# Optimization experiments

Measured on AMD Instinct MI355X. Metric: run time of the kernel, lower is better.

The kernel has to match this reference:

```python
import jax, jax.numpy as jnp
import numpy as np

SH_DEGREE = 4
SH_DIM = (SH_DEGREE + 1) ** 2  # 25
SCALE_MIN, SCALE_MAX = 0.01, 100.0
SCALE_PCT = 0.1
SRF, GPP = 1, 1


def sh_basis(d):
    # Real spherical harmonics up to l=4 for unit directions d (..., 3) -> (..., 25)
    x, y, z = d[..., 0], d[..., 1], d[..., 2]
    x2, y2, z2 = x * x, y * y, z * z
    return jnp.stack([
        jnp.full_like(x, 0.2820947918),
        0.4886025119 * y, 0.4886025119 * z, 0.4886025119 * x,
        1.0925484306 * x * y, 1.0925484306 * y * z, 0.3153915653 * (3.0 * z2 - 1.0),
        1.0925484306 * x * z, 0.5462742153 * (x2 - y2),
        0.5900435899 * y * (3.0 * x2 - y2), 2.8906114426 * x * y * z,
        0.4570457995 * y * (5.0 * z2 - 1.0), 0.3731763326 * z * (5.0 * z2 - 3.0),
        0.4570457995 * x * (5.0 * z2 - 1.0), 1.4453057213 * z * (x2 - y2),
        0.5900435899 * x * (x2 - 3.0 * y2),
        2.5033429418 * x * y * (x2 - y2), 1.7701307698 * y * z * (3.0 * x2 - y2),
        0.9461746958 * x * y * (7.0 * z2 - 1.0), 0.6690465436 * y * z * (7.0 * z2 - 3.0),
        0.1057855469 * (35.0 * z2 * z2 - 30.0 * z2 + 3.0),
        0.6690465436 * x * z * (7.0 * z2 - 3.0),
        0.4730873479 * (x2 - y2) * (7.0 * z2 - 1.0),
        1.7701307698 * x * z * (x2 - 3.0 * y2),
        0.6258357354 * (x2 * x2 - 6.0 * x2 * y2 + y2 * y2),
    ], -1)


# Fixed sample directions + inverse basis matrices for per-band SH rotation (Wigner-D via sampling)
_rng = np.random.default_rng(0)
_SAMPLES, _YS_INV = {}, {}
for _l in range(1, SH_DEGREE + 1):
    _v = _rng.normal(size=(2 * _l + 1, 3))
    _v /= np.linalg.norm(_v, axis=-1, keepdims=True)
    _SAMPLES[_l] = _v.astype(np.float32)
    _B = np.asarray(sh_basis(jnp.asarray(_SAMPLES[_l])))[:, _l * _l:(_l + 1) ** 2]  # (n, n) rows=samples
    _YS_INV[_l] = np.linalg.inv(_B.T).astype(np.float32)  # inverse of columns-are-samples matrix


def quat_to_rotmat(q):
    # wxyz convention
    w, x, y, z = q[..., 0], q[..., 1], q[..., 2], q[..., 3]
    r0 = jnp.stack([1 - 2 * (y * y + z * z), 2 * (x * y - w * z), 2 * (x * z + w * y)], -1)
    r1 = jnp.stack([2 * (x * y + w * z), 1 - 2 * (x * x + z * z), 2 * (y * z - w * x)], -1)
    r2 = jnp.stack([2 * (x * z - w * y), 2 * (y * z + w * x), 1 - 2 * (x * x + y * y)], -1)
    return jnp.stack([r0, r1, r2], -2)


def rotate_sh(sh, R_c2w):
    # sh: (B,V,R,srf,gpp,3,25); R_c2w: (B,V,3,3). Block-diagonal per-band rotation.
    outs = [sh[..., :1]]  # l=0 invariant
    for l in range(1, SH_DEGREE + 1):
        lo, hi = l * l, (l + 1) ** 2
        S = jnp.asarray(_SAMPLES[l])  # (n,3)
        drot = jnp.einsum('bvji,nj->bvni', R_c2w, S)  # R^T d_n
        Yrot = jnp.swapaxes(sh_basis(drot)[..., lo:hi], -1, -2)  # (B,V,n,n) columns=samples
        D = jnp.swapaxes(Yrot @ jnp.asarray(_YS_INV[l]), -1, -2)  # coefficient rotation
        outs.append(jnp.einsum('bvmn,bvrsgxn->bvrsgxm', D, sh[..., lo:hi]))
    return jnp.concatenate(outs, -1)


def setup_inputs() -> dict:
    key = jax.random.key(0)
    ks = jax.random.split(key, 8)
    B, V, H, W = 2, 4, 256, 256
    R = H * W
    C = 3 + 4 + 3 * SH_DIM  # 82
    pre_gaussians = jax.random.normal(ks[0], (B, V, R, SRF, C), jnp.float32)
    pixel_centers = jax.random.uniform(ks[1], (B, V, R, SRF, 2), jnp.float32)
    q = jax.random.normal(ks[2], (B, V, 4), jnp.float32)
    q = q / jnp.linalg.norm(q, axis=-1, keepdims=True)
    Rm = quat_to_rotmat(q)
    t = 0.5 * jax.random.normal(ks[3], (B, V, 3), jnp.float32)
    E = jnp.zeros((B, V, 4, 4), jnp.float32)
    E = E.at[..., :3, :3].set(Rm).at[..., :3, 3].set(t).at[..., 3, 3].set(1.0)
    f = 1.0 + 0.2 * jax.random.uniform(ks[4], (B, V, 2), jnp.float32)
    c = 0.5 + 0.02 * jax.random.normal(ks[5], (B, V, 2), jnp.float32)
    K = jnp.zeros((B, V, 3, 3), jnp.float32)
    K = K.at[..., 0, 0].set(f[..., 0]).at[..., 1, 1].set(f[..., 1])
    K = K.at[..., 0, 2].set(c[..., 0]).at[..., 1, 2].set(c[..., 1]).at[..., 2, 2].set(1.0)
    opacities = jax.random.uniform(ks[6], (B, V, R), jnp.float32)
    depths = 0.5 + 9.5 * jax.random.uniform(ks[7], (B, V, R), jnp.float32)
    return {"pre_gaussians": pre_gaussians, "pixel_centers": pixel_centers,
            "extrinsics": E, "intrinsics": K, "opacities": opacities,
            "depths": depths, "img_h": H, "img_w": W}


def reference(pre_gaussians, pixel_centers, extrinsics, intrinsics, opacities, depths, img_h, img_w):
    H, W = img_h, img_w
    B, V, R = pre_gaussians.shape[:3]
    C = pre_gaussians.shape[-1]
    pg = jnp.broadcast_to(pre_gaussians[..., None, :], (B, V, R, SRF, GPP, C))
    pc = jnp.broadcast_to(pixel_centers[..., None, :], (B, V, R, SRF, GPP, 2))
    op = jnp.broadcast_to(opacities[..., None, None], (B, V, R, SRF, GPP))
    dep = jnp.broadcast_to(depths[..., None, None], (B, V, R, SRF, GPP))
    scales_raw, quats, sh = pg[..., :3], pg[..., 3:7], pg[..., 7:]
    scales = (SCALE_MIN + (SCALE_MAX - SCALE_MIN) * jax.nn.sigmoid(scales_raw)) * dep[..., None]
    pixel_size = jnp.array([1.0 / W, 1.0 / H], jnp.float32)
    K2inv = jnp.linalg.inv(intrinsics[..., :2, :2])
    scale_adj = SCALE_PCT * jnp.einsum('bvij,j->bv', K2inv, pixel_size)
    scales = scales * scale_adj[:, :, None, None, None, None]
    quats = quats / jnp.linalg.norm(quats, axis=-1, keepdims=True)
    R_w2c = extrinsics[..., :3, :3]
    R_c2w = jnp.swapaxes(R_w2c, -1, -2)
    Rq = quat_to_rotmat(quats)
    cov = jnp.einsum('...ik,...k,...jk->...ij', Rq, scales * scales, Rq)  # Rq S S^T Rq^T
    cov = jnp.einsum('bvai,bvrsgij,bvcj->bvrsgac', R_c2w, cov, R_c2w)
    Kinv = jnp.linalg.inv(intrinsics)
    xy1 = jnp.concatenate([pc, jnp.ones_like(pc[..., :1])], -1)
    dir_cam = jnp.einsum('bvij,bvrsgj->bvrsgi', Kinv, xy1)
    dir_cam = dir_cam / jnp.linalg.norm(dir_cam, axis=-1, keepdims=True)
    ray_d = jnp.einsum('bvij,bvrsgj->bvrsgi', R_c2w, dir_cam)
    t = extrinsics[..., :3, 3]
    cam_o = -jnp.einsum('bvij,bvj->bvi', R_c2w, t)  # camera center in world
    ray_o = jnp.broadcast_to(cam_o[:, :, None, None, None, :], ray_d.shape)
    means = ray_o + ray_d * dep[..., None]
    sh = sh.reshape(B, V, R, SRF, GPP, 3, SH_DIM)
    sh = rotate_sh(sh, R_c2w)
    return (means, scales, cov, quats, op, sh)
```

## Files before the change

kernel.cpp:

```cpp
#include <hip/hip_runtime.h>

#define VSZ  192
#define TILE 64
#define NTHR 256
#define IN_F  (TILE * 82)
#define SEC_M  0
#define SEC_S  192
#define SEC_C  384
#define SEC_Q  960
#define SEC_O  1216
#define SEC_SH 1280
#define OUT_F  6080

__device__ __forceinline__ void sh_basis25(float x, float y, float z, float* Y) {
    float x2 = x * x, y2 = y * y, z2 = z * z;
    Y[0]  = 0.2820947918f;
    Y[1]  = 0.4886025119f * y;
    Y[2]  = 0.4886025119f * z;
    Y[3]  = 0.4886025119f * x;
    Y[4]  = 1.0925484306f * x * y;
    Y[5]  = 1.0925484306f * y * z;
    Y[6]  = 0.3153915653f * (3.0f * z2 - 1.0f);
    Y[7]  = 1.0925484306f * x * z;
    Y[8]  = 0.5462742153f * (x2 - y2);
    Y[9]  = 0.5900435899f * y * (3.0f * x2 - y2);
    Y[10] = 2.8906114426f * x * y * z;
    Y[11] = 0.4570457995f * y * (5.0f * z2 - 1.0f);
    Y[12] = 0.3731763326f * z * (5.0f * z2 - 3.0f);
    Y[13] = 0.4570457995f * x * (5.0f * z2 - 1.0f);
    Y[14] = 1.4453057213f * z * (x2 - y2);
    Y[15] = 0.5900435899f * x * (x2 - 3.0f * y2);
    Y[16] = 2.5033429418f * x * y * (x2 - y2);
    Y[17] = 1.7701307698f * y * z * (3.0f * x2 - y2);
    Y[18] = 0.9461746958f * x * y * (7.0f * z2 - 1.0f);
    Y[19] = 0.6690465436f * y * z * (7.0f * z2 - 3.0f);
    Y[20] = 0.1057855469f * (35.0f * z2 * z2 - 30.0f * z2 + 3.0f);
    Y[21] = 0.6690465436f * x * z * (7.0f * z2 - 3.0f);
    Y[22] = 0.4730873479f * (x2 - y2) * (7.0f * z2 - 1.0f);
    Y[23] = 1.7701307698f * x * z * (x2 - 3.0f * y2);
    Y[24] = 0.6258357354f * (x2 * x2 - 6.0f * x2 * y2 + y2 * y2);
}

__global__ __launch_bounds__(64) void setup_kernel(
        const float* __restrict__ ext,
        const float* __restrict__ intr,
        const int* __restrict__ ph,
        const int* __restrict__ pw,
        float* __restrict__ vdg) {
    __shared__ float Bs[24][9];
    __shared__ float Yrs[24][9];
    __shared__ float normInv[24];

    int bv = blockIdx.x;
    int tid = threadIdx.x;
    const float* E = ext + bv * 16;
    const float* K = intr + bv * 9;
    float* o = vdg + bv * VSZ;

    const float z0 = 0.5f, r0 = 0.8660254037844386f;
    const float TWO_PI = 6.283185307179586f;

    if (tid < 24) {
        int l, base;
        if      (tid < 3)  { l = 1; base = 0;  }
        else if (tid < 8)  { l = 2; base = 3;  }
        else if (tid < 15) { l = 3; base = 8;  }
        else               { l = 4; base = 15; }
        int n  = 2 * l + 1;
        int si = tid - base;
        int lo = l * l;
        float phs = 0.4f + TWO_PI * (float)si / (float)n;
        float sx = r0 * cosf(phs), sy = r0 * sinf(phs), sz = z0;
        float Y[25];
        sh_basis25(sx, sy, sz, Y);
        for (int k = 0; k < n; k++) Bs[tid][k] = Y[lo + k];
        float dx = E[0] * sx + E[1] * sy + E[2]  * sz;
        float dy = E[4] * sx + E[5] * sy + E[6]  * sz;
        float dz = E[8] * sx + E[9] * sy + E[10] * sz;
        sh_basis25(dx, dy, dz, Y);
        for (int k = 0; k < n; k++) Yrs[tid][k] = Y[lo + k];
    }
    __syncthreads();

    if (tid < 24) {
        int l, base;
        if      (tid < 3)  { l = 1; base = 0;  }
        else if (tid < 8)  { l = 2; base = 3;  }
        else if (tid < 15) { l = 3; base = 8;  }
        else               { l = 4; base = 15; }
        int n = 2 * l + 1;
        int m = tid - base;
        float acc = 0.f;
        for (int s = 0; s < n; s++) { float v = Bs[base + s][m]; acc += v * v; }
        normInv[tid] = 1.0f / acc;
    }
    __syncthreads();

    const int dofs[5] = {0, 22, 31, 56, 105};
    for (int e = tid; e < 164; e += 64) {
        int l, ebase, sbase;
        if      (e < 9)  { l = 1; ebase = 0;  sbase = 0;  }
        else if (e < 34) { l = 2; ebase = 9;  sbase = 3;  }
        else if (e < 83) { l = 3; ebase = 34; sbase = 8;  }
        else             { l = 4; ebase = 83; sbase = 15; }
        int n = 2 * l + 1;
        int el = e - ebase;
        int m = el / n, k = el % n;
        float acc = 0.f;
        for (int s = 0; s < n; s++) acc += Yrs[sbase + s][k] * Bs[sbase + s][m];
        o[dofs[l] + m * n + k] = acc * normInv[sbase + m];
    }

    if (tid == 0) {
        float Rw2c[3][3], Rc2w[3][3], t[3];
        for (int i = 0; i < 3; i++) {
            for (int j = 0; j < 3; j++) Rw2c[i][j] = E[i * 4 + j];
            t[i] = E[i * 4 + 3];
        }
        for (int i = 0; i < 3; i++)
            for (int j = 0; j < 3; j++) Rc2w[i][j] = Rw2c[j][i];
        for (int i = 0; i < 3; i++)
            for (int j = 0; j < 3; j++) o[i * 3 + j] = Rc2w[i][j];
        for (int i = 0; i < 3; i++) {
            float s = 0.f;
            for (int j = 0; j < 3; j++) s += Rc2w[i][j] * t[j];
            o[9 + i] = -s;
        }
        float a = K[0], b = K[1], c = K[2], d = K[3], e = K[4], f = K[5],
              g = K[6], h = K[7], ii = K[8];
        float det = a * (e * ii - f * h) - b * (d * ii - f * g) + c * (d * h - e * g);
        float id = 1.0f / det;
        o[12 + 0] = (e * ii - f * h) * id; o[12 + 1] = (c * h - b * ii) * id; o[12 + 2] = (b * f - c * e) * id;
        o[12 + 3] = (f * g - d * ii) * id; o[12 + 4] = (a * ii - c * g) * id; o[12 + 5] = (c * d - a * f) * id;
        o[12 + 6] = (d * h - e * g) * id; o[12 + 7] = (b * g - a * h) * id; o[12 + 8] = (a * e - b * d) * id;
        float det2 = a * e - b * d;
        float i00 = e / det2, i01 = -b / det2, i10 = -d / det2, i11 = a / det2;
        float ps0 = 1.0f / (float)(*pw), ps1 = 1.0f / (float)(*ph);
        o[21] = 0.1f * ((i00 + i10) * ps0 + (i01 + i11) * ps1);
    }
}

template <int NB>
__device__ __forceinline__ void apply_D(const float* __restrict__ D,
                                        const float* __restrict__ si,
                                        float* __restrict__ so) {
#pragma unroll
    for (int m = 0; m < NB; m++) {
        float acc = 0.f;
#pragma unroll
        for (int k = 0; k < NB; k++) acc += D[m * NB + k] * si[k];
        so[m] = acc;
    }
}

__global__ __launch_bounds__(NTHR, 6) void adapter_kernel(
    const float* __restrict__ pg, const float* __restrict__ pc,
    const float* __restrict__ ops, const float* __restrict__ deps,
    const float* __restrict__ vdg, float* __restrict__ out,
    int R, long long N)
{
    __shared__ __align__(16) float tile[OUT_F];
    __shared__ float vd[VSZ];

    int bv = blockIdx.y;
    long long tilebase = (long long)bv * R + (long long)blockIdx.x * TILE;
    int cnt = R - blockIdx.x * TILE;
    if (cnt > TILE) cnt = TILE;
    bool full = (cnt == TILE);

    for (int i = threadIdx.x; i < 186; i += NTHR) vd[i] = vdg[bv * VSZ + i];

    const float* src = pg + tilebase * 82;
    if (full) {
        const float4* s4 = (const float4*)src;
        float4* t4 = (float4*)tile;
        for (int e = threadIdx.x; e < IN_F / 4; e += NTHR) t4[e] = s4[e];
    } else {
        for (int ff = threadIdx.x; ff < cnt * 82; ff += NTHR) tile[ff] = src[ff];
    }
    __syncthreads();

    int rec = threadIdx.x & 63;
    int sub = threadIdx.x >> 6;
    bool active = rec < cnt;
    long long g = tilebase + rec;
    const float* row = tile + rec * 82;

    float gin[7];
    float depth = 0.f, opac = 0.f, px = 0.f, py = 0.f;
    float si[25];

    if (sub == 0) {
        if (active) {
#pragma unroll
            for (int i = 0; i < 7; i++) gin[i] = row[i];
            depth = deps[g];
            opac  = ops[g];
            float2 pxy = ((const float2*)pc)[g];
            px = pxy.x; py = pxy.y;
        }
    } else {
        if (active) {
            int cb = 7 + 25 * (sub - 1);
#pragma unroll
            for (int m = 0; m < 25; m++) si[m] = row[cb + m];
        }
    }
    __syncthreads();

    if (sub == 0) {
        if (active) {
            float sadj = vd[21];
            float sc[3];
#pragma unroll
            for (int i = 0; i < 3; i++) {
                float sg = 1.0f / (1.0f + expf(-gin[i]));
                sc[i] = (0.01f + 99.99f * sg) * depth * sadj;
            }
            float qw = gin[3], qx = gin[4], qy = gin[5], qz = gin[6];
            float qn = rsqrtf(qw * qw + qx * qx + qy * qy + qz * qz);
            qw *= qn; qx *= qn; qy *= qn; qz *= qn;
            float Rq[3][3];
            Rq[0][0] = 1.f - 2.f * (qy * qy + qz * qz);
            Rq[0][1] = 2.f * (qx * qy - qw * qz);
            Rq[0][2] = 2.f * (qx * qz + qw * qy);
            Rq[1][0] = 2.f * (qx * qy + qw * qz);
            Rq[1][1] = 1.f - 2.f * (qx * qx + qz * qz);
            Rq[1][2] = 2.f * (qy * qz - qw * qx);
            Rq[2][0] = 2.f * (qx * qz - qw * qy);
            Rq[2][1] = 2.f * (qy * qz + qw * qx);
            Rq[2][2] = 1.f - 2.f * (qx * qx + qy * qy);

            float Rc[3][3];
#pragma unroll
            for (int i = 0; i < 3; i++)
#pragma unroll
                for (int j = 0; j < 3; j++) Rc[i][j] = vd[i * 3 + j];

            float A[3][3];
#pragma unroll
            for (int i = 0; i < 3; i++)
#pragma unroll
                for (int k = 0; k < 3; k++)
                    A[i][k] = Rc[i][0] * Rq[0][k] + Rc[i][1] * Rq[1][k] + Rc[i][2] * Rq[2][k];
            float s2[3] = {sc[0] * sc[0], sc[1] * sc[1], sc[2] * sc[2]};

            float dx = vd[12] * px + vd[13] * py + vd[14];
            float dy = vd[15] * px + vd[16] * py + vd[17];
            float dz = vd[18] * px + vd[19] * py + vd[20];
            float dn = rsqrtf(dx * dx + dy * dy + dz * dz);
            dx *= dn; dy *= dn; dz *= dn;
            float rdx = Rc[0][0] * dx + Rc[0][1] * dy + Rc[0][2] * dz;
            float rdy = Rc[1][0] * dx + Rc[1][1] * dy + Rc[1][2] * dz;
            float rdz = Rc[2][0] * dx + Rc[2][1] * dy + Rc[2][2] * dz;

            tile[SEC_M + 3 * rec + 0] = vd[9]  + rdx * depth;
            tile[SEC_M + 3 * rec + 1] = vd[10] + rdy * depth;
            tile[SEC_M + 3 * rec + 2] = vd[11] + rdz * depth;
            tile[SEC_S + 3 * rec + 0] = sc[0];
            tile[SEC_S + 3 * rec + 1] = sc[1];
            tile[SEC_S + 3 * rec + 2] = sc[2];
#pragma unroll
            for (int i = 0; i < 3; i++)
#pragma unroll
                for (int j = 0; j < 3; j++)
                    tile[SEC_C + 9 * rec + i * 3 + j] =
                        A[i][0] * s2[0] * A[j][0] + A[i][1] * s2[1] * A[j][1] + A[i][2] * s2[2] * A[j][2];
            ((float4*)(tile + SEC_Q))[rec] = make_float4(qw, qx, qy, qz);
            tile[SEC_O + rec] = opac;
        }
    } else {
        if (active) {
            float so[25];
            so[0] = si[0];
            apply_D<3>(vd + 22,  si + 1,  so + 1);
            apply_D<5>(vd + 31,  si + 4,  so + 4);
            apply_D<7>(vd + 56,  si + 9,  so + 9);
            apply_D<9>(vd + 105, si + 16, so + 16);
            float* dstsh = tile + SEC_SH + 75 * rec + 25 * (sub - 1);
#pragma unroll
            for (int m = 0; m < 25; m++) dstsh[m] = so[m];
        }
    }
    __syncthreads();

    if (full) {
        const float4* t4 = (const float4*)tile;
        float4* dm  = (float4*)(out +           3 * tilebase);
        float4* ds  = (float4*)(out +  3 * N +  3 * tilebase);
        float4* dc  = (float4*)(out +  6 * N +  9 * tilebase);
        float4* dq  = (float4*)(out + 15 * N +  4 * tilebase);
        float4* dop = (float4*)(out + 19 * N +      tilebase);
        float4* dsh = (float4*)(out + 20 * N + 75 * tilebase);
        int tid = threadIdx.x;
        if (tid < 48)  dm[tid]  = t4[SEC_M / 4 + tid];
        if (tid < 48)  ds[tid]  = t4[SEC_S / 4 + tid];
        for (int e = tid; e < 144; e += NTHR) dc[e] = t4[SEC_C / 4 + e];
        if (tid < 64)  dq[tid]  = t4[SEC_Q / 4 + tid];
        if (tid < 16)  dop[tid] = t4[SEC_O / 4 + tid];
        for (int e = tid; e < 1200; e += NTHR) dsh[e] = t4[SEC_SH / 4 + e];
    } else {
        int tid = threadIdx.x;
        float* dm  = out +           3 * tilebase;
        float* ds  = out +  3 * N +  3 * tilebase;
        float* dc  = out +  6 * N +  9 * tilebase;
        float* dq  = out + 15 * N +  4 * tilebase;
        float* dop = out + 19 * N +      tilebase;
        float* dsh = out + 20 * N + 75 * tilebase;
        for (int e = tid; e < cnt * 3;  e += NTHR) dm[e]  = tile[SEC_M + e];
        for (int e = tid; e < cnt * 3;  e += NTHR) ds[e]  = tile[SEC_S + e];
        for (int e = tid; e < cnt * 9;  e += NTHR) dc[e]  = tile[SEC_C + e];
        for (int e = tid; e < cnt * 4;  e += NTHR) dq[e]  = tile[SEC_Q + e];
        for (int e = tid; e < cnt;      e += NTHR) dop[e] = tile[SEC_O + e];
        for (int e = tid; e < cnt * 75; e += NTHR) dsh[e] = tile[SEC_SH + e];
    }
}

extern "C" void kernel_launch(void* const* d_in, const int* in_sizes, int n_in,
                              void* d_out, int out_size, void* d_ws, size_t ws_size,
                              hipStream_t stream) {
    const float* pg   = (const float*)d_in[0];
    const float* pc   = (const float*)d_in[1];
    const float* ext  = (const float*)d_in[2];
    const float* intr = (const float*)d_in[3];
    const float* ops  = (const float*)d_in[4];
    const float* dep  = (const float*)d_in[5];
    const int*   ph   = (const int*)d_in[6];
    const int*   pw   = (const int*)d_in[7];

    int BV = in_sizes[2] / 16;
    long long N = (long long)in_sizes[4];
    int R = (int)(N / BV);

    float* vd = (float*)d_ws;
    setup_kernel<<<BV, 64, 0, stream>>>(ext, intr, ph, pw, vd);

    dim3 grid((R + TILE - 1) / TILE, BV);
    adapter_kernel<<<grid, NTHR, 0, stream>>>(pg, pc, ops, dep, vd, (float*)d_out, R, N);
}
```

Baseline: 93.84 us.

## Make blocks persistent over four tiles with async global-to-LDS prefetch

Each block now processes four consecutive tiles. The next tile's input is fetched straight into LDS with global_load_lds while the current tile is computed and written out, and the input and output staging buffers are separated so the prefetch cannot clobber results. The intent is to hide global load latency and cut block launch count. In exchange the grid is four times smaller, which lowers parallelism, and LDS per block grows, which may reduce occupancy.

```diff
diff --git a/kernel.cpp b/kernel.cpp
--- a/kernel.cpp
+++ b/kernel.cpp
@@ -1,8 +1,10 @@
 #include <hip/hip_runtime.h>
+#include <stdint.h>
 
 #define VSZ  192
 #define TILE 64
 #define NTHR 256
+#define NT   4
 #define IN_F  (TILE * 82)
 #define SEC_M  0
 #define SEC_S  192
@@ -11,6 +13,12 @@
 #define SEC_O  1216
 #define SEC_SH 1280
 #define OUT_F  6080
+
+typedef const __attribute__((address_space(1))) uint32_t* gas_ptr;
+typedef __attribute__((address_space(3))) uint32_t* las_ptr;
+__device__ __forceinline__ void g2lds16(const float4* g, float4* l) {
+    __builtin_amdgcn_global_load_lds((gas_ptr)(const void*)g, (las_ptr)(void*)l, 16, 0, 0);
+}
 
 __device__ __forceinline__ void sh_basis25(float x, float y, float z, float* Y) {
     float x2 = x * x, y2 = y * y, z2 = z * z;
@@ -153,166 +161,198 @@
     }
 }
 
-__global__ __launch_bounds__(NTHR, 6) void adapter_kernel(
+__global__ __launch_bounds__(NTHR) void adapter_kernel(
     const float* __restrict__ pg, const float* __restrict__ pc,
     const float* __restrict__ ops, const float* __restrict__ deps,
     const float* __restrict__ vdg, float* __restrict__ out,
-    int R, long long N)
+    int R, long long N, int tilesPerView)
 {
-    __shared__ __align__(16) float tile[OUT_F];
+    __shared__ __align__(16) float inb[IN_F];
+    __shared__ __align__(16) float ob[OUT_F];
     __shared__ float vd[VSZ];
 
     int bv = blockIdx.y;
-    long long tilebase = (long long)bv * R + (long long)blockIdx.x * TILE;
-    int cnt = R - blockIdx.x * TILE;
-    if (cnt > TILE) cnt = TILE;
-    bool full = (cnt == TILE);
+    int t0 = blockIdx.x * NT;
+    if (t0 >= tilesPerView) return;
 
     for (int i = threadIdx.x; i < 186; i += NTHR) vd[i] = vdg[bv * VSZ + i];
 
-    const float* src = pg + tilebase * 82;
-    if (full) {
-        const float4* s4 = (const float4*)src;
-        float4* t4 = (float4*)tile;
-        for (int e = threadIdx.x; e < IN_F / 4; e += NTHR) t4[e] = s4[e];
-    } else {
-        for (int ff = threadIdx.x; ff < cnt * 82; ff += NTHR) tile[ff] = src[ff];
-    }
-    __syncthreads();
-
-    int rec = threadIdx.x & 63;
-    int sub = threadIdx.x >> 6;
-    bool active = rec < cnt;
-    long long g = tilebase + rec;
-    const float* row = tile + rec * 82;
-
-    float gin[7];
-    float depth = 0.f, opac = 0.f, px = 0.f, py = 0.f;
-    float si[25];
-
-    if (sub == 0) {
-        if (active) {
-#pragma unroll
-            for (int i = 0; i < 7; i++) gin[i] = row[i];
-            depth = deps[g];
-            opac  = ops[g];
-            float2 pxy = ((const float2*)pc)[g];
-            px = pxy.x; py = pxy.y;
-        }
-    } else {
-        if (active) {
-            int cb = 7 + 25 * (sub - 1);
-#pragma unroll
-            for (int m = 0; m < 25; m++) si[m] = row[cb + m];
-        }
-    }
-    __syncthreads();
-
-    if (sub == 0) {
-        if (active) {
-            float sadj = vd[21];
-            float sc[3];
-#pragma unroll
-            for (int i = 0; i < 3; i++) {
-                float sg = 1.0f / (1.0f + expf(-gin[i]));
-                sc[i] = (0.01f + 99.99f * sg) * depth * sadj;
-            }
-            float qw = gin[3], qx = gin[4], qy = gin[5], qz = gin[6];
-            float qn = rsqrtf(qw * qw + qx * qx + qy * qy + qz * qz);
-            qw *= qn; qx *= qn; qy *= qn; qz *= qn;
-            float Rq[3][3];
-            Rq[0][0] = 1.f - 2.f * (qy * qy + qz * qz);
-            Rq[0][1] = 2.f * (qx * qy - qw * qz);
-            Rq[0][2] = 2.f * (qx * qz + qw * qy);
-            Rq[1][0] = 2.f * (qx * qy + qw * qz);
-            Rq[1][1] = 1.f - 2.f * (qx * qx + qz * qz);
-            Rq[1][2] = 2.f * (qy * qz - qw * qx);
-            Rq[2][0] = 2.f * (qx * qz - qw * qy);
-            Rq[2][1] = 2.f * (qy * qz + qw * qx);
-            Rq[2][2] = 1.f - 2.f * (qx * qx + qy * qy);
-
-            float Rc[3][3];
-#pragma unroll
-            for (int i = 0; i < 3; i++)
-#pragma unroll
-                for (int j = 0; j < 3; j++) Rc[i][j] = vd[i * 3 + j];
-
-            float A[3][3];
-#pragma unroll
-            for (int i = 0; i < 3; i++)
-#pragma unroll
-                for (int k = 0; k < 3; k++)
-                    A[i][k] = Rc[i][0] * Rq[0][k] + Rc[i][1] * Rq[1][k] + Rc[i][2] * Rq[2][k];
-            float s2[3] = {sc[0] * sc[0], sc[1] * sc[1], sc[2] * sc[2]};
-
-            float dx = vd[12] * px + vd[13] * py + vd[14];
-            float dy = vd[15] * px + vd[16] * py + vd[17];
-            float dz = vd[18] * px + vd[19] * py + vd[20];
-            float dn = rsqrtf(dx * dx + dy * dy + dz * dz);
-            dx *= dn; dy *= dn; dz *= dn;
-            float rdx = Rc[0][0] * dx + Rc[0][1] * dy + Rc[0][2] * dz;
-            float rdy = Rc[1][0] * dx + Rc[1][1] * dy + Rc[1][2] * dz;
-            float rdz = Rc[2][0] * dx + Rc[2][1] * dy + Rc[2][2] * dz;
-
-            tile[SEC_M + 3 * rec + 0] = vd[9]  + rdx * depth;
-            tile[SEC_M + 3 * rec + 1] = vd[10] + rdy * depth;
-            tile[SEC_M + 3 * rec + 2] = vd[11] + rdz * depth;
-            tile[SEC_S + 3 * rec + 0] = sc[0];
-            tile[SEC_S + 3 * rec + 1] = sc[1];
-            tile[SEC_S + 3 * rec + 2] = sc[2];
-#pragma unroll
-            for (int i = 0; i < 3; i++)
-#pragma unroll
-                for (int j = 0; j < 3; j++)
-                    tile[SEC_C + 9 * rec + i * 3 + j] =
-                        A[i][0] * s2[0] * A[j][0] + A[i][1] * s2[1] * A[j][1] + A[i][2] * s2[2] * A[j][2];
-            ((float4*)(tile + SEC_Q))[rec] = make_float4(qw, qx, qy, qz);
-            tile[SEC_O + rec] = opac;
-        }
-    } else {
-        if (active) {
-            float so[25];
-            so[0] = si[0];
-            apply_D<3>(vd + 22,  si + 1,  so + 1);
-            apply_D<5>(vd + 31,  si + 4,  so + 4);
-            apply_D<7>(vd + 56,  si + 9,  so + 9);
-            apply_D<9>(vd + 105, si + 16, so + 16);
-            float* dstsh = tile + SEC_SH + 75 * rec + 25 * (sub - 1);
-#pragma unroll
-            for (int m = 0; m < 25; m++) dstsh[m] = so[m];
-        }
-    }
-    __syncthreads();
-
-    if (full) {
-        const float4* t4 = (const float4*)tile;
-        float4* dm  = (float4*)(out +           3 * tilebase);
-        float4* ds  = (float4*)(out +  3 * N +  3 * tilebase);
-        float4* dc  = (float4*)(out +  6 * N +  9 * tilebase);
-        float4* dq  = (float4*)(out + 15 * N +  4 * tilebase);
-        float4* dop = (float4*)(out + 19 * N +      tilebase);
-        float4* dsh = (float4*)(out + 20 * N + 75 * tilebase);
-        int tid = threadIdx.x;
-        if (tid < 48)  dm[tid]  = t4[SEC_M / 4 + tid];
-        if (tid < 48)  ds[tid]  = t4[SEC_S / 4 + tid];
-        for (int e = tid; e < 144; e += NTHR) dc[e] = t4[SEC_C / 4 + e];
-        if (tid < 64)  dq[tid]  = t4[SEC_Q / 4 + tid];
-        if (tid < 16)  dop[tid] = t4[SEC_O / 4 + tid];
-        for (int e = tid; e < 1200; e += NTHR) dsh[e] = t4[SEC_SH / 4 + e];
-    } else {
-        int tid = threadIdx.x;
-        float* dm  = out +           3 * tilebase;
-        float* ds  = out +  3 * N +  3 * tilebase;
-        float* dc  = out +  6 * N +  9 * tilebase;
-        float* dq  = out + 15 * N +  4 * tilebase;
-        float* dop = out + 19 * N +      tilebase;
-        float* dsh = out + 20 * N + 75 * tilebase;
-        for (int e = tid; e < cnt * 3;  e += NTHR) dm[e]  = tile[SEC_M + e];
-        for (int e = tid; e < cnt * 3;  e += NTHR) ds[e]  = tile[SEC_S + e];
-        for (int e = tid; e < cnt * 9;  e += NTHR) dc[e]  = tile[SEC_C + e];
-        for (int e = tid; e < cnt * 4;  e += NTHR) dq[e]  = tile[SEC_Q + e];
-        for (int e = tid; e < cnt;      e += NTHR) dop[e] = tile[SEC_O + e];
-        for (int e = tid; e < cnt * 75; e += NTHR) dsh[e] = tile[SEC_SH + e];
+    {
+        long long tb = (long long)bv * R + (long long)t0 * TILE;
+        int c = R - t0 * TILE; if (c > TILE) c = TILE;
+        const float* src = pg + tb * 82;
+        if (c == TILE) {
+            const float4* s4 = (const float4*)src;
+            float4* i4 = (float4*)inb;
+            int tid = threadIdx.x;
+#pragma unroll
+            for (int k = 0; k < 5; k++) { int e = k * NTHR + tid; g2lds16(s4 + e, i4 + e); }
+            if (tid < IN_F / 4 - 5 * NTHR) { int e = 5 * NTHR + tid; g2lds16(s4 + e, i4 + e); }
+        } else {
+            for (int ff = threadIdx.x; ff < c * 82; ff += NTHR) inb[ff] = src[ff];
+        }
+    }
+
+    for (int it = 0; it < NT; it++) {
+        int t = t0 + it;
+        if (t >= tilesPerView) break;
+        long long tilebase = (long long)bv * R + (long long)t * TILE;
+        int cnt = R - t * TILE; if (cnt > TILE) cnt = TILE;
+        bool full = (cnt == TILE);
+
+        asm volatile("s_waitcnt vmcnt(0)" ::: "memory");
+        __syncthreads();
+
+        int rec = threadIdx.x & 63;
+        int sub = threadIdx.x >> 6;
+        bool active = rec < cnt;
+        long long g = tilebase + rec;
+        const float* row = inb + rec * 82;
+
+        float gin[7];
+        float depth = 0.f, opac = 0.f, px = 0.f, py = 0.f;
+        float si[25];
+
+        if (sub == 0) {
+            if (active) {
+#pragma unroll
+                for (int i = 0; i < 7; i++) gin[i] = row[i];
+                depth = deps[g];
+                opac  = ops[g];
+                float2 pxy = ((const float2*)pc)[g];
+                px = pxy.x; py = pxy.y;
+            }
+        } else {
+            if (active) {
+                int cb = 7 + 25 * (sub - 1);
+#pragma unroll
+                for (int m = 0; m < 25; m++) si[m] = row[cb + m];
+            }
+        }
+        __syncthreads();
+
+        if (it + 1 < NT && t + 1 < tilesPerView) {
+            long long tb = (long long)bv * R + (long long)(t + 1) * TILE;
+            int c = R - (t + 1) * TILE; if (c > TILE) c = TILE;
+            const float* src = pg + tb * 82;
+            if (c == TILE) {
+                const float4* s4 = (const float4*)src;
+                float4* i4 = (float4*)inb;
+                int tid = threadIdx.x;
+#pragma unroll
+                for (int k = 0; k < 5; k++) { int e = k * NTHR + tid; g2lds16(s4 + e, i4 + e); }
+                if (tid < IN_F / 4 - 5 * NTHR) { int e = 5 * NTHR + tid; g2lds16(s4 + e, i4 + e); }
+            } else {
+                for (int ff = threadIdx.x; ff < c * 82; ff += NTHR) inb[ff] = src[ff];
+            }
+        }
+
+        if (sub == 0) {
+            if (active) {
+                float sadj = vd[21];
+                float sc[3];
+#pragma unroll
+                for (int i = 0; i < 3; i++) {
+                    float sg = 1.0f / (1.0f + expf(-gin[i]));
+                    sc[i] = (0.01f + 99.99f * sg) * depth * sadj;
+                }
+                float qw = gin[3], qx = gin[4], qy = gin[5], qz = gin[6];
+                float qn = rsqrtf(qw * qw + qx * qx + qy * qy + qz * qz);
+                qw *= qn; qx *= qn; qy *= qn; qz *= qn;
+                float Rq[3][3];
+                Rq[0][0] = 1.f - 2.f * (qy * qy + qz * qz);
+                Rq[0][1] = 2.f * (qx * qy - qw * qz);
+                Rq[0][2] = 2.f * (qx * qz + qw * qy);
+                Rq[1][0] = 2.f * (qx * qy + qw * qz);
+                Rq[1][1] = 1.f - 2.f * (qx * qx + qz * qz);
+                Rq[1][2] = 2.f * (qy * qz - qw * qx);
+                Rq[2][0] = 2.f * (qx * qz - qw * qy);
+                Rq[2][1] = 2.f * (qy * qz + qw * qx);
+                Rq[2][2] = 1.f - 2.f * (qx * qx + qy * qy);
+
+                float Rc[3][3];
+#pragma unroll
+                for (int i = 0; i < 3; i++)
+#pragma unroll
+                    for (int j = 0; j < 3; j++) Rc[i][j] = vd[i * 3 + j];
+
+                float A[3][3];
+#pragma unroll
+                for (int i = 0; i < 3; i++)
+#pragma unroll
+                    for (int k = 0; k < 3; k++)
+                        A[i][k] = Rc[i][0] * Rq[0][k] + Rc[i][1] * Rq[1][k] + Rc[i][2] * Rq[2][k];
+                float s2[3] = {sc[0] * sc[0], sc[1] * sc[1], sc[2] * sc[2]};
+
+                float dx = vd[12] * px + vd[13] * py + vd[14];
+                float dy = vd[15] * px + vd[16] * py + vd[17];
+                float dz = vd[18] * px + vd[19] * py + vd[20];
+                float dn = rsqrtf(dx * dx + dy * dy + dz * dz);
+                dx *= dn; dy *= dn; dz *= dn;
+                float rdx = Rc[0][0] * dx + Rc[0][1] * dy + Rc[0][2] * dz;
+                float rdy = Rc[1][0] * dx + Rc[1][1] * dy + Rc[1][2] * dz;
+                float rdz = Rc[2][0] * dx + Rc[2][1] * dy + Rc[2][2] * dz;
+
+                ob[SEC_M + 3 * rec + 0] = vd[9]  + rdx * depth;
+                ob[SEC_M + 3 * rec + 1] = vd[10] + rdy * depth;
+                ob[SEC_M + 3 * rec + 2] = vd[11] + rdz * depth;
+                ob[SEC_S + 3 * rec + 0] = sc[0];
+                ob[SEC_S + 3 * rec + 1] = sc[1];
+                ob[SEC_S + 3 * rec + 2] = sc[2];
+#pragma unroll
+                for (int i = 0; i < 3; i++)
+#pragma unroll
+                    for (int j = 0; j < 3; j++)
+                        ob[SEC_C + 9 * rec + i * 3 + j] =
+                            A[i][0] * s2[0] * A[j][0] + A[i][1] * s2[1] * A[j][1] + A[i][2] * s2[2] * A[j][2];
+                ((float4*)(ob + SEC_Q))[rec] = make_float4(qw, qx, qy, qz);
+                ob[SEC_O + rec] = opac;
+            }
+        } else {
+            if (active) {
+                float so[25];
+                so[0] = si[0];
+                apply_D<3>(vd + 22,  si + 1,  so + 1);
+                apply_D<5>(vd + 31,  si + 4,  so + 4);
+                apply_D<7>(vd + 56,  si + 9,  so + 9);
+                apply_D<9>(vd + 105, si + 16, so + 16);
+                float* dstsh = ob + SEC_SH + 75 * rec + 25 * (sub - 1);
+#pragma unroll
+                for (int m = 0; m < 25; m++) dstsh[m] = so[m];
+            }
+        }
+        __syncthreads();
+
+        if (full) {
+            const float4* t4 = (const float4*)ob;
+            float4* dm  = (float4*)(out +           3 * tilebase);
+            float4* ds  = (float4*)(out +  3 * N +  3 * tilebase);
+            float4* dc  = (float4*)(out +  6 * N +  9 * tilebase);
+            float4* dq  = (float4*)(out + 15 * N +  4 * tilebase);
+            float4* dop = (float4*)(out + 19 * N +      tilebase);
+            float4* dsh = (float4*)(out + 20 * N + 75 * tilebase);
+            int tid = threadIdx.x;
+            if (tid < 48)  dm[tid]  = t4[SEC_M / 4 + tid];
+            if (tid < 48)  ds[tid]  = t4[SEC_S / 4 + tid];
+            for (int e = tid; e < 144; e += NTHR) dc[e] = t4[SEC_C / 4 + e];
+            if (tid < 64)  dq[tid]  = t4[SEC_Q / 4 + tid];
+            if (tid < 16)  dop[tid] = t4[SEC_O / 4 + tid];
+            for (int e = tid; e < 1200; e += NTHR) dsh[e] = t4[SEC_SH / 4 + e];
+        } else {
+            int tid = threadIdx.x;
+            float* dm  = out +           3 * tilebase;
+            float* ds  = out +  3 * N +  3 * tilebase;
+            float* dc  = out +  6 * N +  9 * tilebase;
+            float* dq  = out + 15 * N +  4 * tilebase;
+            float* dop = out + 19 * N +      tilebase;
+            float* dsh = out + 20 * N + 75 * tilebase;
+            for (int e = tid; e < cnt * 3;  e += NTHR) dm[e]  = ob[SEC_M + e];
+            for (int e = tid; e < cnt * 3;  e += NTHR) ds[e]  = ob[SEC_S + e];
+            for (int e = tid; e < cnt * 9;  e += NTHR) dc[e]  = ob[SEC_C + e];
+            for (int e = tid; e < cnt * 4;  e += NTHR) dq[e]  = ob[SEC_Q + e];
+            for (int e = tid; e < cnt;      e += NTHR) dop[e] = ob[SEC_O + e];
+            for (int e = tid; e < cnt * 75; e += NTHR) dsh[e] = ob[SEC_SH + e];
+        }
     }
 }
 
@@ -335,6 +375,7 @@
     float* vd = (float*)d_ws;
     setup_kernel<<<BV, 64, 0, stream>>>(ext, intr, ph, pw, vd);
 
-    dim3 grid((R + TILE - 1) / TILE, BV);
-    adapter_kernel<<<grid, NTHR, 0, stream>>>(pg, pc, ops, dep, vd, (float*)d_out, R, N);
-}
+    int tiles = (R + TILE - 1) / TILE;
+    dim3 grid((tiles + NT - 1) / NT, BV);
+    adapter_kernel<<<grid, NTHR, 0, stream>>>(pg, pc, ops, dep, vd, (float*)d_out, R, N, tiles);
+}
```

Measured after the change: 94.16 us. About the same (+0.3%).
